# Optimization experiments

Hardware: AMD Instinct MI355X
Metric: run time of the kernel (lower is better)

Reference implementation:

```python
import jax, jax.numpy as jnp
import numpy as np

B, N, DH = 8, 2048, 512
EPS = 1e-5


def _layer_norm(x, g, b):
    m = x.mean(-1, keepdims=True)
    v = ((x - m) ** 2).mean(-1, keepdims=True)
    return (x - m) * jax.lax.rsqrt(v + EPS) * g + b


def setup_inputs() -> dict:
    key = jax.random.key(0)
    ks = jax.random.split(key, 20)
    s = 1.0 / np.sqrt(DH)
    sf = 1.0 / np.sqrt(2 * DH)
    return {
        "H": jax.random.normal(ks[0], (B, N, DH), jnp.float32),
        "adj": jax.random.uniform(ks[1], (B, N, N), jnp.float32),
        "hop_emb": jax.random.normal(ks[2], (N, DH), jnp.float32),
        "Wq": jax.random.normal(ks[3], (DH, DH), jnp.float32) * s,
        "bq": jnp.zeros((DH,), jnp.float32),
        "Wk": jax.random.normal(ks[4], (DH, DH), jnp.float32) * s,
        "bk": jnp.zeros((DH,), jnp.float32),
        "Wv": jax.random.normal(ks[5], (DH, DH), jnp.float32) * s,
        "bv": jnp.zeros((DH,), jnp.float32),
        "W1": jax.random.normal(ks[6], (DH, 2 * DH), jnp.float32) * s,
        "b1": jnp.zeros((2 * DH,), jnp.float32),
        "W2": jax.random.normal(ks[7], (2 * DH, DH), jnp.float32) * sf,
        "b2": jnp.zeros((DH,), jnp.float32),
        "g1": jnp.ones((DH,), jnp.float32),
        "be1": jnp.zeros((DH,), jnp.float32),
        "g2": jnp.ones((DH,), jnp.float32),
        "be2": jnp.zeros((DH,), jnp.float32),
    }


def reference(H, adj, hop_emb, Wq, bq, Wk, bk, Wv, bv, W1, b1, W2, b2, g1, be1, g2, be2):
    Q = H @ Wq + bq                                     # [B,N,DH]
    K = H @ Wk + bk
    V = H @ Wv + bv
    scores = jnp.einsum("bid,bjd->bij", Q, K) / np.sqrt(DH).astype(np.float32)
    # (adj[...,None] * hop_emb).mean(-1) == adj * hop_emb.mean(-1)[j]
    hop_effect = adj * hop_emb.mean(-1)[None, None, :]  # [B,N,N]
    attn = jax.nn.softmax(scores * hop_effect, axis=-1)
    attn_out = jnp.einsum("bij,bjd->bid", attn, V)
    x = _layer_norm(attn_out + H, g1, be1)
    ffn = jax.nn.relu(x @ W1 + b1) @ W2 + b2
    return _layer_norm(ffn + x, g2, be2)
```

## Files before the change

### kernel.cpp

```cpp
#include <hip/hip_runtime.h>

typedef unsigned short u16;
typedef __bf16 bf16x8 __attribute__((ext_vector_type(8)));
typedef float f32x4 __attribute__((ext_vector_type(4)));

#define SEQN 2048
#define DHID 512

static __device__ __forceinline__ float bf2f(u16 u) {
    union { unsigned int i; float f; } c; c.i = ((unsigned int)u) << 16; return c.f;
}
static __device__ __forceinline__ u16 f2bf(float f) {
    union { float f; unsigned int i; } c; c.f = f;
    unsigned int x = c.i;
    return (u16)((x + 0x7fffu + ((x >> 16) & 1u)) >> 16);
}

static __device__ __forceinline__ void gld_lds16(const u16* g, u16* l) {
    __builtin_amdgcn_global_load_lds(
        (__attribute__((address_space(1))) void*)(g),
        (__attribute__((address_space(3))) void*)(l), 16, 0, 0);
}

__global__ __launch_bounds__(256) void cvt_kernel(const float* __restrict__ src,
                                                  u16* __restrict__ dst, int n) {
    int i = (blockIdx.x * 256 + threadIdx.x) * 8;
    if (i >= n) return;
    float4 a = *(const float4*)(src + i);
    float4 b = *(const float4*)(src + i + 4);
    union { uint4 u; u16 s[8]; } o;
    o.s[0] = f2bf(a.x); o.s[1] = f2bf(a.y); o.s[2] = f2bf(a.z); o.s[3] = f2bf(a.w);
    o.s[4] = f2bf(b.x); o.s[5] = f2bf(b.y); o.s[6] = f2bf(b.z); o.s[7] = f2bf(b.w);
    *(uint4*)(dst + i) = o.u;
}

__global__ __launch_bounds__(256) void cvt_t_kernel(const float* __restrict__ src,
                                                    u16* __restrict__ dst, int K, int N) {
    int idx = blockIdx.x * 256 + threadIdx.x;
    if (idx >= K * N) return;
    int n = idx / K, k = idx - n * K;
    dst[idx] = f2bf(src[(size_t)k * N + n]);
}

__global__ void hmean_kernel(const float* __restrict__ hop, float* __restrict__ hm) {
    int j = blockIdx.x, t = threadIdx.x;
    const float* p = hop + (size_t)j * DHID + t * 8;
    float4 a = *(const float4*)p;
    float4 b = *(const float4*)(p + 4);
    float s = a.x + a.y + a.z + a.w + b.x + b.y + b.z + b.w;
#pragma unroll
    for (int m = 1; m < 64; m <<= 1) s += __shfl_xor(s, m);
    if (t == 0) hm[j] = s * (1.0f / (float)DHID);
}

enum { EPI_BIAS = 0, EPI_RELU = 1, EPI_PLAIN = 3, EPI_BIAS_T = 4, EPI_QKV = 5 };

template <int EPI>
__global__ __launch_bounds__(256) void gemm_bt(
    const u16* __restrict__ A, const u16* __restrict__ Bt, u16* __restrict__ C,
    const float* __restrict__ bias,
    int K, int lda, int ldb, int ldc,
    u16* __restrict__ Qo, u16* __restrict__ Ko, u16* __restrict__ Vto,
    const float* __restrict__ bq_, const float* __restrict__ bk_,
    const float* __restrict__ bv_)
{
    __shared__ u16 As[128 * 32];
    __shared__ u16 Bs[128 * 32];

    const int tid = threadIdx.x;
    const u16* Ab = A;
    const u16* Bb = Bt;

    const int bm0 = blockIdx.y * 128, bn0 = blockIdx.x * 128;
    const int wid = tid >> 6, lane = tid & 63, quad = lane >> 4, l16 = lane & 15;
    const int wm = (wid >> 1) * 64, wn = (wid & 1) * 64;
    const int srow = lane >> 2;
    const int skof = (lane & 3) * 8;

    f32x4 acc[4][4];
#pragma unroll
    for (int i = 0; i < 4; ++i)
#pragma unroll
        for (int j = 0; j < 4; ++j) acc[i][j] = (f32x4){0.f, 0.f, 0.f, 0.f};

    for (int k0 = 0; k0 < K; k0 += 32) {
#pragma unroll
        for (int it = 0; it < 2; ++it) {
            int c = wid * 2 + it;
            gld_lds16(Ab + (size_t)(bm0 + c * 16 + srow) * lda + k0 + skof,
                      &As[c * 512]);
        }
#pragma unroll
        for (int it = 0; it < 2; ++it) {
            int c = wid * 2 + it;
            gld_lds16(Bb + (size_t)(bn0 + c * 16 + srow) * ldb + k0 + skof,
                      &Bs[c * 512]);
        }
        __syncthreads();

        bf16x8 af[4], bfr[4];
#pragma unroll
        for (int i = 0; i < 4; ++i)
            af[i] = *(const bf16x8*)&As[(wm + i * 16 + l16) * 32 + quad * 8];
#pragma unroll
        for (int j = 0; j < 4; ++j)
            bfr[j] = *(const bf16x8*)&Bs[(wn + j * 16 + l16) * 32 + quad * 8];
#pragma unroll
        for (int i = 0; i < 4; ++i)
#pragma unroll
            for (int j = 0; j < 4; ++j)
                acc[i][j] = __builtin_amdgcn_mfma_f32_16x16x32_bf16(af[i], bfr[j], acc[i][j], 0, 0, 0);
        __syncthreads();
    }

#pragma unroll
    for (int i = 0; i < 4; ++i) {
#pragma unroll
        for (int j = 0; j < 4; ++j) {
            const int gn = bn0 + wn + j * 16 + l16;
            const int gm0 = bm0 + wm + i * 16 + quad * 4;
            if constexpr (EPI == EPI_BIAS || EPI == EPI_RELU) {
                const float b = bias[gn];
#pragma unroll
                for (int r = 0; r < 4; ++r) {
                    float v = acc[i][j][r] + b;
                    if constexpr (EPI == EPI_RELU) v = fmaxf(v, 0.f);
                    C[(size_t)(gm0 + r) * ldc + gn] = f2bf(v);
                }
            } else if constexpr (EPI == EPI_BIAS_T) {
                const float b = bias[gn];
                const int bb = gm0 >> 11, n = gm0 & 2047;
                ushort4 o;
                o.x = f2bf(acc[i][j][0] + b);
                o.y = f2bf(acc[i][j][1] + b);
                o.z = f2bf(acc[i][j][2] + b);
                o.w = f2bf(acc[i][j][3] + b);
                *(ushort4*)&C[((size_t)bb * 512 + gn) * 2048 + n] = o;
            } else if constexpr (EPI == EPI_QKV) {
                const int sel = gn >> 9;
                const int n = gn & 511;
                if (sel == 0) {
                    const float b = bq_[n];
#pragma unroll
                    for (int r = 0; r < 4; ++r)
                        Qo[(size_t)(gm0 + r) * DHID + n] = f2bf(acc[i][j][r] + b);
                } else if (sel == 1) {
                    const float b = bk_[n];
#pragma unroll
                    for (int r = 0; r < 4; ++r)
                        Ko[(size_t)(gm0 + r) * DHID + n] = f2bf(acc[i][j][r] + b);
                } else {
                    const float b = bv_[n];
                    const int bb = gm0 >> 11, nn2 = gm0 & 2047;
                    ushort4 o;
                    o.x = f2bf(acc[i][j][0] + b);
                    o.y = f2bf(acc[i][j][1] + b);
                    o.z = f2bf(acc[i][j][2] + b);
                    o.w = f2bf(acc[i][j][3] + b);
                    *(ushort4*)&Vto[((size_t)bb * 512 + n) * 2048 + nn2] = o;
                }
            } else {
#pragma unroll
                for (int r = 0; r < 4; ++r)
                    C[(size_t)(gm0 + r) * ldc + gn] = f2bf(acc[i][j][r]);
            }
        }
    }
}

__global__ __launch_bounds__(256, 1) void attn_kernel(
    const u16* __restrict__ Q, const u16* __restrict__ K, const u16* __restrict__ Vt,
    const float* __restrict__ adj, const float* __restrict__ hm,
    u16* __restrict__ Opart, float* __restrict__ Lpart)
{
    extern __shared__ u16 lds[];
    u16* Ks = lds;
    u16* Vs = lds + 16384;

    const int tid = threadIdx.x, wid = tid >> 6, lane = tid & 63;
    const int quad = lane >> 4, l16 = lane & 15;
    const int b = blockIdx.x;
    const int q0w = blockIdx.y * 64 + wid * 16;
    const int z = blockIdx.z;
    const int srow = lane >> 2, sko = (lane & 3) * 8;

    const u16* Qg = Q + (size_t)b * SEQN * DHID;
    const u16* Kg = K + (size_t)b * SEQN * DHID;
    const u16* Vg = Vt + (size_t)b * DHID * SEQN;
    const float* adjg = adj + (size_t)b * SEQN * SEQN;
    u16* Og = Opart + ((size_t)z * 8 + b) * SEQN * DHID;
    u16* Plds = lds + wid * 640;

    const float scale = 0.044194173824159216f;

    bf16x8 qf[16];
#pragma unroll
    for (int ds = 0; ds < 16; ++ds)
        qf[ds] = *(const bf16x8*)(Qg + (size_t)(q0w + l16) * DHID + ds * 32 + quad * 8);

    f32x4 oacc[32];
#pragma unroll
    for (int dt = 0; dt < 32; ++dt) oacc[dt] = (f32x4){0.f, 0.f, 0.f, 0.f};
    float lsum[4] = {0.f, 0.f, 0.f, 0.f};

    for (int kt = 0; kt < 32; ++kt) {
        const int kv0 = z * 1024 + kt * 32;

#pragma unroll
        for (int i = 0; i < 8; ++i) {
            int id = wid * 8 + i;
            int ds = id >> 1, c = id & 1;
            gld_lds16(Kg + (size_t)(kv0 + c * 16 + srow) * DHID + ds * 32 + sko,
                      &Ks[ds * 1024 + c * 512]);
        }
        __syncthreads();

#pragma unroll
        for (int i = 0; i < 8; ++i) {
            int id = wid * 8 + i;
            gld_lds16(Vg + (size_t)(id * 16 + srow) * SEQN + kv0 + sko,
                      &Vs[id * 512]);
        }

        float hv0 = hm[kv0 + l16] * scale;
        float hv1 = hm[kv0 + 16 + l16] * scale;
        float av[8];
        const float* arow = adjg + (size_t)(q0w + quad * 4) * SEQN + kv0;
#pragma unroll
        for (int r = 0; r < 4; ++r) {
            av[r]     = arow[(size_t)r * SEQN + l16];
            av[4 + r] = arow[(size_t)r * SEQN + 16 + l16];
        }

        f32x4 s0a = {0.f,0.f,0.f,0.f}, s0b = {0.f,0.f,0.f,0.f};
        f32x4 s1a = {0.f,0.f,0.f,0.f}, s1b = {0.f,0.f,0.f,0.f};
#pragma unroll
        for (int ds = 0; ds < 16; ds += 2) {
            bf16x8 k00 = *(const bf16x8*)&Ks[ds * 1024 + l16 * 32 + quad * 8];
            bf16x8 k01 = *(const bf16x8*)&Ks[ds * 1024 + 512 + l16 * 32 + quad * 8];
            s0a = __builtin_amdgcn_mfma_f32_16x16x32_bf16(qf[ds], k00, s0a, 0, 0, 0);
            s1a = __builtin_amdgcn_mfma_f32_16x16x32_bf16(qf[ds], k01, s1a, 0, 0, 0);
            bf16x8 k10 = *(const bf16x8*)&Ks[(ds + 1) * 1024 + l16 * 32 + quad * 8];
            bf16x8 k11 = *(const bf16x8*)&Ks[(ds + 1) * 1024 + 512 + l16 * 32 + quad * 8];
            s0b = __builtin_amdgcn_mfma_f32_16x16x32_bf16(qf[ds + 1], k10, s0b, 0, 0, 0);
            s1b = __builtin_amdgcn_mfma_f32_16x16x32_bf16(qf[ds + 1], k11, s1b, 0, 0, 0);
        }
        f32x4 s0 = s0a + s0b, s1 = s1a + s1b;
        __syncthreads();

#pragma unroll
        for (int r = 0; r < 4; ++r) {
            float p0 = __expf(s0[r] * av[r] * hv0);
            float p1 = __expf(s1[r] * av[4 + r] * hv1);
            lsum[r] += p0 + p1;
            Plds[(quad * 4 + r) * 40 + l16] = f2bf(p0);
            Plds[(quad * 4 + r) * 40 + 16 + l16] = f2bf(p1);
        }
        asm volatile("s_waitcnt lgkmcnt(0)" ::: "memory");

        bf16x8 pf = *(const bf16x8*)&Plds[l16 * 40 + quad * 8];
#pragma unroll
        for (int dt = 0; dt < 32; ++dt) {
            bf16x8 vf = *(const bf16x8*)&Vs[(dt * 16 + l16) * 32 + quad * 8];
            oacc[dt] = __builtin_amdgcn_mfma_f32_16x16x32_bf16(pf, vf, oacc[dt], 0, 0, 0);
        }
        __syncthreads();
    }

#pragma unroll
    for (int r = 0; r < 4; ++r) {
#pragma unroll
        for (int m = 1; m < 16; m <<= 1) lsum[r] += __shfl_xor(lsum[r], m);
        if (l16 == 0)
            Lpart[(size_t)z * 16384 + b * 2048 + q0w + quad * 4 + r] = lsum[r];
    }
#pragma unroll
    for (int dt = 0; dt < 32; ++dt) {
#pragma unroll
        for (int r = 0; r < 4; ++r) {
            Og[(size_t)(q0w + quad * 4 + r) * DHID + dt * 16 + l16] =
                f2bf(oacc[dt][r]);
        }
    }
}

__global__ __launch_bounds__(256) void ln_comb_kernel(
    const u16* __restrict__ O1, const u16* __restrict__ O2,
    const float* __restrict__ L1, const float* __restrict__ L2,
    const float* __restrict__ Hf,
    const float* __restrict__ g, const float* __restrict__ be,
    u16* __restrict__ out)
{
    size_t row = blockIdx.x;
    int t = threadIdx.x, wid = t >> 6, lane = t & 63;
    float sc = 1.f / (L1[row] + L2[row]);

    unsigned int a1 = *(const unsigned int*)(O1 + row * (size_t)DHID + t * 2);
    unsigned int a2 = *(const unsigned int*)(O2 + row * (size_t)DHID + t * 2);
    float2 h = *(const float2*)(Hf + row * (size_t)DHID + t * 2);
    float x0 = (bf2f((u16)(a1 & 0xffff)) + bf2f((u16)(a2 & 0xffff))) * sc + h.x;
    float x1 = (bf2f((u16)(a1 >> 16)) + bf2f((u16)(a2 >> 16))) * sc + h.y;

    float s = x0 + x1, sq = x0 * x0 + x1 * x1;
#pragma unroll
    for (int m = 1; m < 64; m <<= 1) { s += __shfl_xor(s, m); sq += __shfl_xor(sq, m); }
    __shared__ float rs[4], rq[4];
    if (lane == 0) { rs[wid] = s; rq[wid] = sq; }
    __syncthreads();
    s = rs[0] + rs[1] + rs[2] + rs[3];
    sq = rq[0] + rq[1] + rq[2] + rq[3];
    float mean = s * (1.f / (float)DHID);
    float var = sq * (1.f / (float)DHID) - mean * mean;
    float rstd = rsqrtf(var + 1e-5f);

    float2 vg = *(const float2*)(g + t * 2);
    float2 vbe = *(const float2*)(be + t * 2);
    float y0 = (x0 - mean) * rstd * vg.x + vbe.x;
    float y1 = (x1 - mean) * rstd * vg.y + vbe.y;
    unsigned int o = (unsigned int)f2bf(y0) | ((unsigned int)f2bf(y1) << 16);
    *(unsigned int*)(out + row * (size_t)DHID + t * 2) = o;
}

__global__ __launch_bounds__(256) void ln_kernel_f32out(
    const u16* __restrict__ a, const u16* __restrict__ bp,
    const float* __restrict__ g, const float* __restrict__ be,
    float* __restrict__ out)
{
    size_t row = blockIdx.x;
    int t = threadIdx.x, wid = t >> 6, lane = t & 63;
    unsigned int va = *(const unsigned int*)(a + row * (size_t)DHID + t * 2);
    unsigned int vb = *(const unsigned int*)(bp + row * (size_t)DHID + t * 2);
    float x0 = bf2f((u16)(va & 0xffff)) + bf2f((u16)(vb & 0xffff));
    float x1 = bf2f((u16)(va >> 16)) + bf2f((u16)(vb >> 16));
    float s = x0 + x1, sq = x0 * x0 + x1 * x1;
#pragma unroll
    for (int m = 1; m < 64; m <<= 1) { s += __shfl_xor(s, m); sq += __shfl_xor(sq, m); }
    __shared__ float rs[4], rq[4];
    if (lane == 0) { rs[wid] = s; rq[wid] = sq; }
    __syncthreads();
    s = rs[0] + rs[1] + rs[2] + rs[3];
    sq = rq[0] + rq[1] + rq[2] + rq[3];
    float mean = s * (1.f / (float)DHID);
    float var = sq * (1.f / (float)DHID) - mean * mean;
    float rstd = rsqrtf(var + 1e-5f);
    float2 vg = *(const float2*)(g + t * 2);
    float2 vbe = *(const float2*)(be + t * 2);
    float y0 = (x0 - mean) * rstd * vg.x + vbe.x;
    float y1 = (x1 - mean) * rstd * vg.y + vbe.y;
    *(float2*)(out + row * (size_t)DHID + t * 2) = make_float2(y0, y1);
}

extern "C" void kernel_launch(void* const* d_in, const int* in_sizes, int n_in,
                              void* d_out, int out_size, void* d_ws, size_t ws_size,
                              hipStream_t stream) {
    const float* H   = (const float*)d_in[0];
    const float* adj = (const float*)d_in[1];
    const float* hop = (const float*)d_in[2];
    const float* Wq  = (const float*)d_in[3];
    const float* bq  = (const float*)d_in[4];
    const float* Wk  = (const float*)d_in[5];
    const float* bk  = (const float*)d_in[6];
    const float* Wv  = (const float*)d_in[7];
    const float* bv  = (const float*)d_in[8];
    const float* W1  = (const float*)d_in[9];
    const float* b1  = (const float*)d_in[10];
    const float* W2  = (const float*)d_in[11];
    const float* b2  = (const float*)d_in[12];
    const float* g1  = (const float*)d_in[13];
    const float* be1 = (const float*)d_in[14];
    const float* g2  = (const float*)d_in[15];
    const float* be2 = (const float*)d_in[16];

    const size_t MiB = 1ull << 20;
    char* w = (char*)d_ws;
    float* hm   = (float*)w;
    float* Lp   = (float*)(w + 256 * 1024);
    u16* Hb    = (u16*)(w + 1 * MiB);
    u16* Wqkvt = (u16*)(w + 17 * MiB);
    u16* W1t   = (u16*)(w + 18 * MiB + 512 * 1024);
    u16* W2t   = (u16*)(w + 19 * MiB + 512 * 1024);
    u16* Q     = (u16*)(w + 21 * MiB);
    u16* Kb    = (u16*)(w + 37 * MiB);
    u16* Vt    = (u16*)(w + 53 * MiB);
    u16* O1    = (u16*)(w + 69 * MiB);
    u16* O2    = (u16*)(w + 85 * MiB);
    u16* HID   = (u16*)(w + 101 * MiB);
    u16* X   = Kb;
    u16* F2  = Vt;

    const int BN = 8, N = SEQN, D = DHID;

    cvt_kernel<<<(BN * N * D) / (8 * 256), 256, 0, stream>>>(H, Hb, BN * N * D);
    cvt_t_kernel<<<(D * D + 255) / 256, 256, 0, stream>>>(Wq, Wqkvt, D, D);
    cvt_t_kernel<<<(D * D + 255) / 256, 256, 0, stream>>>(Wk, Wqkvt + D * D, D, D);
    cvt_t_kernel<<<(D * D + 255) / 256, 256, 0, stream>>>(Wv, Wqkvt + 2 * D * D, D, D);
    cvt_t_kernel<<<(D * 2 * D + 255) / 256, 256, 0, stream>>>(W1, W1t, D, 2 * D);
    cvt_t_kernel<<<(2 * D * D + 255) / 256, 256, 0, stream>>>(W2, W2t, 2 * D, D);

    hmean_kernel<<<N, 64, 0, stream>>>(hop, hm);

    gemm_bt<EPI_QKV><<<dim3(12, 128, 1), 256, 0, stream>>>(
        Hb, Wqkvt, nullptr, nullptr, D, D, D, 0, Q, Kb, Vt, bq, bk, bv);

    attn_kernel<<<dim3(8, 32, 2), 256, 65536, stream>>>(
        Q, Kb, Vt, adj, hm, O1, Lp);

    ln_comb_kernel<<<BN * N, 256, 0, stream>>>(
        O1, O2, Lp, Lp + 16384, H, g1, be1, X);

    gemm_bt<EPI_RELU><<<dim3(8, 128, 1), 256, 0, stream>>>(
        X, W1t, HID, b1, D, D, D, 2 * D, nullptr, nullptr, nullptr, nullptr, nullptr, nullptr);

    gemm_bt<EPI_BIAS><<<dim3(4, 128, 1), 256, 0, stream>>>(
        HID, W2t, F2, b2, 2 * D, 2 * D, 2 * D, D, nullptr, nullptr, nullptr, nullptr, nullptr, nullptr);

    ln_kernel_f32out<<<BN * N, 256, 0, stream>>>(F2, X, g2, be2, (float*)d_out);
}
```

Baseline: 595.5 us.

## Replace split-KV attention with per-wave head-dim split and in-kernel normalization

The attention kernel no longer splits the key range across two blocks and combines the partial results afterwards. Each block now owns 32 query rows over the full key range, and wave pairs split the 512-wide output dimension in halves. Normalization by the softmax sum moves into the kernel, so the layer-norm kernel reads only one bf16 attention output instead of two partials plus sums. This halves the output accumulators and allows two blocks per CU, but each wave pair computes the same QK^T scores twice and each block stages K/V tiles for only 32 query rows.

```diff
diff --git a/kernel.cpp b/kernel.cpp
--- a/kernel.cpp
+++ b/kernel.cpp
@@ -168,10 +168,10 @@
     }
 }
 
-__global__ __launch_bounds__(256, 1) void attn_kernel(
+__global__ __launch_bounds__(256, 2) void attn_kernel(
     const u16* __restrict__ Q, const u16* __restrict__ K, const u16* __restrict__ Vt,
     const float* __restrict__ adj, const float* __restrict__ hm,
-    u16* __restrict__ Opart, float* __restrict__ Lpart)
+    u16* __restrict__ AO)
 {
     extern __shared__ u16 lds[];
     u16* Ks = lds;
@@ -180,15 +180,15 @@
     const int tid = threadIdx.x, wid = tid >> 6, lane = tid & 63;
     const int quad = lane >> 4, l16 = lane & 15;
     const int b = blockIdx.x;
-    const int q0w = blockIdx.y * 64 + wid * 16;
-    const int z = blockIdx.z;
+    const int q0 = blockIdx.y * 32 + (wid >> 1) * 16;
+    const int D0 = (wid & 1) * 256;
     const int srow = lane >> 2, sko = (lane & 3) * 8;
 
     const u16* Qg = Q + (size_t)b * SEQN * DHID;
     const u16* Kg = K + (size_t)b * SEQN * DHID;
     const u16* Vg = Vt + (size_t)b * DHID * SEQN;
     const float* adjg = adj + (size_t)b * SEQN * SEQN;
-    u16* Og = Opart + ((size_t)z * 8 + b) * SEQN * DHID;
+    u16* AOg = AO + (size_t)b * SEQN * DHID;
     u16* Plds = lds + wid * 640;
 
     const float scale = 0.044194173824159216f;
@@ -196,15 +196,15 @@
     bf16x8 qf[16];
 #pragma unroll
     for (int ds = 0; ds < 16; ++ds)
-        qf[ds] = *(const bf16x8*)(Qg + (size_t)(q0w + l16) * DHID + ds * 32 + quad * 8);
-
-    f32x4 oacc[32];
-#pragma unroll
-    for (int dt = 0; dt < 32; ++dt) oacc[dt] = (f32x4){0.f, 0.f, 0.f, 0.f};
+        qf[ds] = *(const bf16x8*)(Qg + (size_t)(q0 + l16) * DHID + ds * 32 + quad * 8);
+
+    f32x4 oacc[16];
+#pragma unroll
+    for (int dt = 0; dt < 16; ++dt) oacc[dt] = (f32x4){0.f, 0.f, 0.f, 0.f};
     float lsum[4] = {0.f, 0.f, 0.f, 0.f};
 
-    for (int kt = 0; kt < 32; ++kt) {
-        const int kv0 = z * 1024 + kt * 32;
+    for (int kt = 0; kt < 64; ++kt) {
+        const int kv0 = kt * 32;
 
 #pragma unroll
         for (int i = 0; i < 8; ++i) {
@@ -225,7 +225,7 @@
         float hv0 = hm[kv0 + l16] * scale;
         float hv1 = hm[kv0 + 16 + l16] * scale;
         float av[8];
-        const float* arow = adjg + (size_t)(q0w + quad * 4) * SEQN + kv0;
+        const float* arow = adjg + (size_t)(q0 + quad * 4) * SEQN + kv0;
 #pragma unroll
         for (int r = 0; r < 4; ++r) {
             av[r]     = arow[(size_t)r * SEQN + l16];
@@ -260,8 +260,8 @@
 
         bf16x8 pf = *(const bf16x8*)&Plds[l16 * 40 + quad * 8];
 #pragma unroll
-        for (int dt = 0; dt < 32; ++dt) {
-            bf16x8 vf = *(const bf16x8*)&Vs[(dt * 16 + l16) * 32 + quad * 8];
+        for (int dt = 0; dt < 16; ++dt) {
+            bf16x8 vf = *(const bf16x8*)&Vs[(D0 + dt * 16 + l16) * 32 + quad * 8];
             oacc[dt] = __builtin_amdgcn_mfma_f32_16x16x32_bf16(pf, vf, oacc[dt], 0, 0, 0);
         }
         __syncthreads();
@@ -271,36 +271,29 @@
     for (int r = 0; r < 4; ++r) {
 #pragma unroll
         for (int m = 1; m < 16; m <<= 1) lsum[r] += __shfl_xor(lsum[r], m);
-        if (l16 == 0)
-            Lpart[(size_t)z * 16384 + b * 2048 + q0w + quad * 4 + r] = lsum[r];
+        lsum[r] = 1.f / lsum[r];
     }
 #pragma unroll
-    for (int dt = 0; dt < 32; ++dt) {
+    for (int dt = 0; dt < 16; ++dt) {
 #pragma unroll
         for (int r = 0; r < 4; ++r) {
-            Og[(size_t)(q0w + quad * 4 + r) * DHID + dt * 16 + l16] =
-                f2bf(oacc[dt][r]);
+            AOg[(size_t)(q0 + quad * 4 + r) * DHID + D0 + dt * 16 + l16] =
+                f2bf(oacc[dt][r] * lsum[r]);
         }
     }
 }
 
-__global__ __launch_bounds__(256) void ln_comb_kernel(
-    const u16* __restrict__ O1, const u16* __restrict__ O2,
-    const float* __restrict__ L1, const float* __restrict__ L2,
-    const float* __restrict__ Hf,
+__global__ __launch_bounds__(256) void ln_hf32_kernel(
+    const u16* __restrict__ a, const float* __restrict__ Hf,
     const float* __restrict__ g, const float* __restrict__ be,
     u16* __restrict__ out)
 {
     size_t row = blockIdx.x;
     int t = threadIdx.x, wid = t >> 6, lane = t & 63;
-    float sc = 1.f / (L1[row] + L2[row]);
-
-    unsigned int a1 = *(const unsigned int*)(O1 + row * (size_t)DHID + t * 2);
-    unsigned int a2 = *(const unsigned int*)(O2 + row * (size_t)DHID + t * 2);
+    unsigned int va = *(const unsigned int*)(a + row * (size_t)DHID + t * 2);
     float2 h = *(const float2*)(Hf + row * (size_t)DHID + t * 2);
-    float x0 = (bf2f((u16)(a1 & 0xffff)) + bf2f((u16)(a2 & 0xffff))) * sc + h.x;
-    float x1 = (bf2f((u16)(a1 >> 16)) + bf2f((u16)(a2 >> 16))) * sc + h.y;
-
+    float x0 = bf2f((u16)(va & 0xffff)) + h.x;
+    float x1 = bf2f((u16)(va >> 16)) + h.y;
     float s = x0 + x1, sq = x0 * x0 + x1 * x1;
 #pragma unroll
     for (int m = 1; m < 64; m <<= 1) { s += __shfl_xor(s, m); sq += __shfl_xor(sq, m); }
@@ -312,7 +305,6 @@
     float mean = s * (1.f / (float)DHID);
     float var = sq * (1.f / (float)DHID) - mean * mean;
     float rstd = rsqrtf(var + 1e-5f);
-
     float2 vg = *(const float2*)(g + t * 2);
     float2 vbe = *(const float2*)(be + t * 2);
     float y0 = (x0 - mean) * rstd * vg.x + vbe.x;
@@ -374,7 +366,6 @@
     const size_t MiB = 1ull << 20;
     char* w = (char*)d_ws;
     float* hm   = (float*)w;
-    float* Lp   = (float*)(w + 256 * 1024);
     u16* Hb    = (u16*)(w + 1 * MiB);
     u16* Wqkvt = (u16*)(w + 17 * MiB);
     u16* W1t   = (u16*)(w + 18 * MiB + 512 * 1024);
@@ -382,9 +373,8 @@
     u16* Q     = (u16*)(w + 21 * MiB);
     u16* Kb    = (u16*)(w + 37 * MiB);
     u16* Vt    = (u16*)(w + 53 * MiB);
-    u16* O1    = (u16*)(w + 69 * MiB);
-    u16* O2    = (u16*)(w + 85 * MiB);
-    u16* HID   = (u16*)(w + 101 * MiB);
+    u16* AO    = (u16*)(w + 69 * MiB);
+    u16* HID   = (u16*)(w + 85 * MiB);
     u16* X   = Kb;
     u16* F2  = Vt;
 
@@ -402,11 +392,9 @@
     gemm_bt<EPI_QKV><<<dim3(12, 128, 1), 256, 0, stream>>>(
         Hb, Wqkvt, nullptr, nullptr, D, D, D, 0, Q, Kb, Vt, bq, bk, bv);
 
-    attn_kernel<<<dim3(8, 32, 2), 256, 65536, stream>>>(
-        Q, Kb, Vt, adj, hm, O1, Lp);
-
-    ln_comb_kernel<<<BN * N, 256, 0, stream>>>(
-        O1, O2, Lp, Lp + 16384, H, g1, be1, X);
+    attn_kernel<<<dim3(8, 64), 256, 65536, stream>>>(Q, Kb, Vt, adj, hm, AO);
+
+    ln_hf32_kernel<<<BN * N, 256, 0, stream>>>(AO, H, g1, be1, X);
 
     gemm_bt<EPI_RELU><<<dim3(8, 128, 1), 256, 0, stream>>>(
         X, W1t, HID, b1, D, D, D, 2 * D, nullptr, nullptr, nullptr, nullptr, nullptr, nullptr);
```

Result: faster. 559.4 us (-6.1%).
